# Kernel tuning notes

Measured on AMD Instinct MI355X. Metric: run time of the kernel, lower is better.

The kernel has to match this reference:

```python
import jax, jax.numpy as jnp
import numpy as np

B, S, D, H = 2, 2048, 1024, 16
HD = D // H
WIN = 32
LN_EPS = 1e-5


def _ln(x, g, b):
    m = jnp.mean(x, axis=-1, keepdims=True)
    v = jnp.mean(jnp.square(x - m), axis=-1, keepdims=True)
    return (x - m) / jnp.sqrt(v + LN_EPS) * g + b


def setup_inputs() -> dict:
    key = jax.random.key(0)
    ks = jax.random.split(key, 12)
    def w(k, shape):
        return jax.random.normal(k, shape, dtype=jnp.float32) * 0.02
    inp = {
        'x': jax.random.normal(ks[0], (B, S, D), dtype=jnp.float32),
        'fq_w': w(ks[1], (D, D)), 'fq_b': jnp.zeros((D,), jnp.float32),
        'fk_w': w(ks[2], (D, D)), 'fk_b': jnp.zeros((D,), jnp.float32),
        'fv_w': w(ks[3], (D, D)), 'fv_b': jnp.zeros((D,), jnp.float32),
        'bq_w': w(ks[4], (D, D)), 'bq_b': jnp.zeros((D,), jnp.float32),
        'bk_w': w(ks[5], (D, D)), 'bk_b': jnp.zeros((D,), jnp.float32),
        'bv_w': w(ks[6], (D, D)), 'bv_b': jnp.zeros((D,), jnp.float32),
        'gate_w': w(ks[7], (2 * D, D)), 'gate_b': jnp.zeros((D,), jnp.float32),
        'gln_g': jnp.ones((D,), jnp.float32), 'gln_b': jnp.zeros((D,), jnp.float32),
        'bstr': jnp.asarray(0.1, jnp.float32),
        'out_w': w(ks[8], (D, D)), 'out_b': jnp.zeros((D,), jnp.float32),
        'ln_g': jnp.ones((D,), jnp.float32), 'ln_b': jnp.zeros((D,), jnp.float32),
    }
    return inp


def _heads(x, w, b):
    # [B,S,D] -> [B,H,S,HD]
    y = x @ w + b
    return y.reshape(B, S, H, HD).transpose(0, 2, 1, 3)


def _merge(x):
    return x.transpose(0, 2, 1, 3).reshape(B, S, D)


def _forward(x, fq_w, fq_b, fk_w, fk_b, fv_w, fv_b,
             bq_w, bq_b, bk_w, bk_b, bv_w, bv_b,
             gate_w, gate_b, gln_g, gln_b, bstr, out_w, out_b, ln_g, ln_b):
    scale = 1.0 / np.sqrt(HD)
    i = jnp.arange(S)
    # --- causal forward attention ---
    Q = _heads(x, fq_w, fq_b); K = _heads(x, fk_w, fk_b); V = _heads(x, fv_w, fv_b)
    scores = jnp.einsum('bhqd,bhkd->bhqk', Q, K) * scale
    causal = i[:, None] >= i[None, :]  # allowed positions
    scores = jnp.where(causal[None, None], scores, -jnp.inf)
    fwd = _merge(jnp.einsum('bhqk,bhkd->bhqd', jax.nn.softmax(scores, axis=-1), V))
    # --- limited-window backward attention (future_context = hidden_states) ---
    Qb = _heads(x, bq_w, bq_b); Kb = _heads(x, bk_w, bk_b); Vb = _heads(x, bv_w, bv_b)
    sb = jnp.einsum('bhqd,bhkd->bhqk', Qb, Kb) * scale
    valid = (i[None, :] > i[:, None]) & (i[None, :] <= i[:, None] + WIN)
    sb = jnp.where(valid[None, None], sb, -jnp.inf)
    # rows with no valid future (last row) get scores reset to 0 -> uniform softmax,
    # matching torch's all_masked handling
    row_valid = valid.any(axis=-1)  # [S]
    sb = jnp.where(row_valid[None, None, :, None], sb, 0.0)
    bwd = _merge(jnp.einsum('bhqk,bhkd->bhqd', jax.nn.softmax(sb, axis=-1), Vb))
    # --- weak gated fusion (eval mode: no dropout, backward detached) ---
    combined = jnp.concatenate([fwd, bwd], axis=-1)
    gate = jax.nn.sigmoid(_ln(combined @ gate_w + gate_b, gln_g, gln_b))
    strength = jax.nn.sigmoid(bstr) * 0.3
    fused = fwd + strength * gate * jax.lax.stop_gradient(bwd)
    out = fused @ out_w + out_b
    return _ln(x + out, ln_g, ln_b)


def reference(x, fq_w, fq_b, fk_w, fk_b, fv_w, fv_b,
              bq_w, bq_b, bk_w, bk_b, bv_w, bv_b,
              gate_w, gate_b, gln_g, gln_b, bstr, out_w, out_b, ln_g, ln_b):
    return _forward(x, fq_w, fq_b, fk_w, fk_b, fv_w, fv_b,
                    bq_w, bq_b, bk_w, bk_b, bv_w, bv_b,
                    gate_w, gate_b, gln_g, gln_b, bstr, out_w, out_b, ln_g, ln_b)
```

## Files before the change

kernel.cpp:

```cpp
#include <hip/hip_runtime.h>

#define S_LEN 2048
#define NH 16
#define HD 64
#define DMODEL 1024
#define NTOK 4096
#define ELTS_PER 4194304
#define QSCALE 0.18033688f

typedef __attribute__((ext_vector_type(8))) __bf16 bfrag;
typedef __attribute__((ext_vector_type(8))) short s8v;
typedef __attribute__((ext_vector_type(4))) float f32x4;

__device__ inline float bf2f(short s) {
  unsigned int u = ((unsigned int)(unsigned short)s) << 16;
  float f;
  __builtin_memcpy(&f, &u, 4);
  return f;
}
__device__ inline short f2bf(float f) {
  unsigned int u;
  __builtin_memcpy(&u, &f, 4);
  u = (u + 0x7fffu + ((u >> 16) & 1u)) >> 16;
  return (short)u;
}
__device__ inline short f2bf_n(float f) {
  __bf16 h = (__bf16)f;
  short s;
  __builtin_memcpy(&s, &h, 2);
  return s;
}
__device__ inline float bflo(unsigned int u) {
  unsigned int t = u << 16;
  float f; __builtin_memcpy(&f, &t, 4); return f;
}
__device__ inline float bfhi(unsigned int u) {
  unsigned int t = u & 0xffff0000u;
  float f; __builtin_memcpy(&f, &t, 4); return f;
}
__device__ __forceinline__ void gll16(const short* g, short* l) {
  __builtin_amdgcn_global_load_lds(
      (const __attribute__((address_space(1))) void*)g,
      (__attribute__((address_space(3))) void*)l, 16, 0, 0);
}

__global__ __launch_bounds__(256) void cvt_bf16_kernel(const float* __restrict__ in,
                                                       short* __restrict__ out, int n) {
  int i = (blockIdx.x * 256 + threadIdx.x) * 4;
  if (i + 3 < n) {
    float4 v = *reinterpret_cast<const float4*>(in + i);
    short4 o;
    o.x = f2bf(v.x); o.y = f2bf(v.y); o.z = f2bf(v.z); o.w = f2bf(v.w);
    *reinterpret_cast<short4*>(out + i) = o;
  }
}

__global__ void transpose_cvt_all(const float* __restrict__ s0, const float* __restrict__ s1,
                                  const float* __restrict__ s2, const float* __restrict__ s3,
                                  const float* __restrict__ s4, const float* __restrict__ s5,
                                  const float* __restrict__ s6, const float* __restrict__ s7,
                                  short* d0, short* d1, short* d2, short* d3,
                                  short* d4, short* d5, short* d6, short* d7) {
  const int z = blockIdx.z;
  const int K = (z == 7) ? 2048 : 1024;
  if (blockIdx.y * 32 >= K) return;
  const float* srcs[8] = {s0, s1, s2, s3, s4, s5, s6, s7};
  short* dsts[8] = {d0, d1, d2, d3, d4, d5, d6, d7};
  const float* in = srcs[z];
  short* out = dsts[z];
  __shared__ float tile[32][33];
  int nb = blockIdx.x * 32, kb = blockIdx.y * 32;
  int tx = threadIdx.x, ty = threadIdx.y;
  for (int j = 0; j < 32; j += 8)
    tile[ty + j][tx] = in[(size_t)(kb + ty + j) * 1024 + nb + tx];
  __syncthreads();
  for (int j = 0; j < 32; j += 8)
    out[(size_t)(nb + ty + j) * K + kb + tx] = f2bf(tile[tx][ty + j]);
}

__global__ __launch_bounds__(256) void gemm_qkv_kernel(
    const short* __restrict__ A, int lda, int K,
    const short* __restrict__ B0, const short* __restrict__ B1, const short* __restrict__ B2,
    const short* __restrict__ B3, const short* __restrict__ B4, const short* __restrict__ B5,
    const float* __restrict__ bias0, const float* __restrict__ bias1,
    const float* __restrict__ bias2, const float* __restrict__ bias3,
    const float* __restrict__ bias4, const float* __restrict__ bias5,
    short* __restrict__ outQ) {
  __shared__ short As[128 * 32];
  __shared__ short Bs[128 * 32];
  const int tid = threadIdx.x;
  const int n0 = blockIdx.x * 128;
  const int m0 = blockIdx.y * 128;
  const short* Bp[6] = {B0, B1, B2, B3, B4, B5};
  const float* biasP[6] = {bias0, bias1, bias2, bias3, bias4, bias5};
  const int nsel = n0 >> 10;
  const short* Bt = Bp[nsel] + (size_t)(n0 & 1023) * K;
  const float* bsel = biasP[nsel];

  const int lane = tid & 63;
  const int w = tid >> 6;
  const int wm = (w >> 1) * 64;
  const int wn = (w & 1) * 64;
  const int lr = lane & 15;
  const int lg = lane >> 4;
  const int gr = lane >> 2;
  const int gs = (((lane & 3) ^ ((gr >> 1) & 3)) * 8);
  const int rsw = (lr >> 1) & 3;

  f32x4 acc[4][4];
  for (int a = 0; a < 4; ++a)
    for (int b = 0; b < 4; ++b) acc[a][b] = {0.f, 0.f, 0.f, 0.f};

  for (int k0 = 0; k0 < K; k0 += 32) {
    __syncthreads();
    const short* Ag = A + (size_t)(m0 + w * 32 + gr) * lda + k0 + gs;
    const short* Bg = Bt + (size_t)(w * 32 + gr) * K + k0 + gs;
    gll16(Ag, &As[(w * 32) * 32]);
    gll16(Ag + (size_t)16 * lda, &As[(w * 32 + 16) * 32]);
    gll16(Bg, &Bs[(w * 32) * 32]);
    gll16(Bg + (size_t)16 * K, &Bs[(w * 32 + 16) * 32]);
    __syncthreads();
    bfrag af[4], bfr[4];
    for (int t = 0; t < 4; ++t) {
      af[t] = *reinterpret_cast<const bfrag*>(&As[(wm + t * 16 + lr) * 32 + ((lg ^ rsw) * 8)]);
      bfr[t] = *reinterpret_cast<const bfrag*>(&Bs[(wn + t * 16 + lr) * 32 + ((lg ^ rsw) * 8)]);
    }
    for (int mt = 0; mt < 4; ++mt)
      for (int nt = 0; nt < 4; ++nt)
        acc[mt][nt] = __builtin_amdgcn_mfma_f32_16x16x32_bf16(af[mt], bfr[nt], acc[mt][nt], 0, 0, 0);
  }

  const float cmul = (nsel == 0 || nsel == 3) ? QSCALE : 1.0f;
  for (int mt = 0; mt < 4; ++mt)
    for (int nt = 0; nt < 4; ++nt) {
      int rowb = m0 + wm + mt * 16 + lg * 4;
      int col = n0 + wn + nt * 16 + lr;
      int nh = col & 1023;
      int hh = nh >> 6, d = nh & 63;
      int bb = rowb >> 11, s0 = rowb & 2047;
      float bv = bsel[nh];
      if (nsel == 2 || nsel == 5) {
        short4 o;
        o.x = f2bf_n(acc[mt][nt][0] + bv);
        o.y = f2bf_n(acc[mt][nt][1] + bv);
        o.z = f2bf_n(acc[mt][nt][2] + bv);
        o.w = f2bf_n(acc[mt][nt][3] + bv);
        *reinterpret_cast<short4*>(
            outQ + (size_t)nsel * ELTS_PER +
            ((size_t)(bb * NH + hh) * HD + d) * S_LEN + s0) = o;
      } else {
        for (int i = 0; i < 4; ++i) {
          float v = (acc[mt][nt][i] + bv) * cmul;
          outQ[(size_t)nsel * ELTS_PER +
               (((size_t)(bb * NH + hh) * S_LEN + (s0 + i)) * HD) + d] = f2bf_n(v);
        }
      }
    }
}

__global__ __launch_bounds__(256) void gemm_ksplit_kernel(
    const short* __restrict__ A0, const short* __restrict__ A1, int lda,
    const short* __restrict__ B, int ldb, int K,
    const float* __restrict__ bias, float* __restrict__ out0, float* __restrict__ out1) {
  __shared__ short As[128 * 32];
  __shared__ short Bs[128 * 32];
  const int tid = threadIdx.x;
  const int n0 = blockIdx.x * 128;
  const int m0 = blockIdx.y * 128;
  const int z = blockIdx.z;
  const short* A = z ? A1 : A0;
  const short* Bt = B + (size_t)n0 * ldb + z * K;
  float* outp = z ? out1 : out0;

  const int lane = tid & 63;
  const int w = tid >> 6;
  const int wm = (w >> 1) * 64;
  const int wn = (w & 1) * 64;
  const int lr = lane & 15;
  const int lg = lane >> 4;
  const int gr = lane >> 2;
  const int gs = (((lane & 3) ^ ((gr >> 1) & 3)) * 8);
  const int rsw = (lr >> 1) & 3;

  f32x4 acc[4][4];
  for (int a = 0; a < 4; ++a)
    for (int b = 0; b < 4; ++b) acc[a][b] = {0.f, 0.f, 0.f, 0.f};

  for (int k0 = 0; k0 < K; k0 += 32) {
    __syncthreads();
    const short* Ag = A + (size_t)(m0 + w * 32 + gr) * lda + k0 + gs;
    const short* Bg = Bt + (size_t)(w * 32 + gr) * ldb + k0 + gs;
    gll16(Ag, &As[(w * 32) * 32]);
    gll16(Ag + (size_t)16 * lda, &As[(w * 32 + 16) * 32]);
    gll16(Bg, &Bs[(w * 32) * 32]);
    gll16(Bg + (size_t)16 * ldb, &Bs[(w * 32 + 16) * 32]);
    __syncthreads();
    bfrag af[4], bfr[4];
    for (int t = 0; t < 4; ++t) {
      af[t] = *reinterpret_cast<const bfrag*>(&As[(wm + t * 16 + lr) * 32 + ((lg ^ rsw) * 8)]);
      bfr[t] = *reinterpret_cast<const bfrag*>(&Bs[(wn + t * 16 + lr) * 32 + ((lg ^ rsw) * 8)]);
    }
    for (int mt = 0; mt < 4; ++mt)
      for (int nt = 0; nt < 4; ++nt)
        acc[mt][nt] = __builtin_amdgcn_mfma_f32_16x16x32_bf16(af[mt], bfr[nt], acc[mt][nt], 0, 0, 0);
  }

  for (int mt = 0; mt < 4; ++mt)
    for (int nt = 0; nt < 4; ++nt)
      for (int i = 0; i < 4; ++i) {
        int row = m0 + wm + mt * 16 + lg * 4 + i;
        int col = n0 + wn + nt * 16 + lr;
        float v = acc[mt][nt][i] + (z == 0 ? bias[col] : 0.f);
        outp[(size_t)row * DMODEL + col] = v;
      }
}

__global__ __launch_bounds__(256) void attn_fwd_kernel(const short* __restrict__ Q,
                                                       const short* __restrict__ Kk,
                                                       const short* __restrict__ VT,
                                                       short* __restrict__ fwd) {
  __shared__ short Ps[4][32 * 72];
  const int tid = threadIdx.x;
  const int lane = tid & 63;
  const int w = tid >> 6;
  const int lr = lane & 15;
  const int lg = lane >> 4;
  const int f = blockIdx.x;
  const int xcd = f & 7;
  const int slot = f >> 3;
  const int bh = xcd * 4 + (slot >> 4);
  const int p = slot & 15;
  const int b = bh >> 4;
  const int h = bh & 15;
  const size_t hb = (size_t)(b * NH + h) * S_LEN * HD;
  short* Pw = Ps[w];

  s8v onesi = {0x3F80, 0x3F80, 0x3F80, 0x3F80, 0x3F80, 0x3F80, 0x3F80, 0x3F80};
  bfrag onesv;
  __builtin_memcpy(&onesv, &onesi, 16);

  const int c = (w < 2) ? (2 * p + w) : (63 - 2 * p - (w - 2));
  const int q0 = c * 32;
  const int ktm = c >> 1;

  bfrag qf[2][2];
  for (int mt = 0; mt < 2; ++mt)
    for (int kc = 0; kc < 2; ++kc)
      qf[mt][kc] = *reinterpret_cast<const bfrag*>(
          Q + hb + (size_t)(q0 + mt * 16 + lr) * HD + kc * 32 + lg * 8);

  f32x4 oacc[2][4];
  for (int mt = 0; mt < 2; ++mt)
    for (int nd = 0; nd < 4; ++nd) oacc[mt][nd] = {0.f, 0.f, 0.f, 0.f};
  f32x4 osum[2];
  osum[0] = {0.f, 0.f, 0.f, 0.f};
  osum[1] = {0.f, 0.f, 0.f, 0.f};

  bfrag ka[4][2];
  for (int nb = 0; nb < 4; ++nb)
    for (int kc = 0; kc < 2; ++kc)
      ka[nb][kc] = *reinterpret_cast<const bfrag*>(
          Kk + hb + (size_t)(nb * 16 + lr) * HD + kc * 32 + lg * 8);

  for (int kt = 0; kt <= ktm; ++kt) {
    bfrag vf[4][2];
    for (int nd = 0; nd < 4; ++nd)
      for (int kc = 0; kc < 2; ++kc)
        vf[nd][kc] = *reinterpret_cast<const bfrag*>(
            VT + hb + (size_t)(nd * 16 + lr) * S_LEN + kt * 64 + kc * 32 + lg * 8);
    f32x4 sv[2][4];
    for (int mt = 0; mt < 2; ++mt)
      for (int nb = 0; nb < 4; ++nb) {
        f32x4 z = {0.f, 0.f, 0.f, 0.f};
        z = __builtin_amdgcn_mfma_f32_16x16x32_bf16(qf[mt][0], ka[nb][0], z, 0, 0, 0);
        sv[mt][nb] = __builtin_amdgcn_mfma_f32_16x16x32_bf16(qf[mt][1], ka[nb][1], z, 0, 0, 0);
      }
    if (kt < ktm) {
      for (int nb = 0; nb < 4; ++nb)
        for (int kc = 0; kc < 2; ++kc)
          ka[nb][kc] = *reinterpret_cast<const bfrag*>(
              Kk + hb + (size_t)((kt + 1) * 64 + nb * 16 + lr) * HD + kc * 32 + lg * 8);
    }
    if (kt == ktm) {
      for (int mt = 0; mt < 2; ++mt)
        for (int nb = 0; nb < 4; ++nb)
          for (int i = 0; i < 4; ++i) {
            int colg = kt * 64 + nb * 16 + lr;
            int rowg = q0 + mt * 16 + lg * 4 + i;
            if (colg > rowg) sv[mt][nb][i] = -1e30f;
          }
    }
    for (int mt = 0; mt < 2; ++mt)
      for (int nb = 0; nb < 4; ++nb)
        for (int i = 0; i < 4; ++i)
          Pw[(mt * 16 + lg * 4 + i) * 72 + nb * 16 + lr] = f2bf_n(exp2f(sv[mt][nb][i]));
    for (int mt = 0; mt < 2; ++mt) {
      bfrag pa0 = *reinterpret_cast<const bfrag*>(&Pw[(mt * 16 + lr) * 72 + lg * 8]);
      bfrag pa1 = *reinterpret_cast<const bfrag*>(&Pw[(mt * 16 + lr) * 72 + 32 + lg * 8]);
      for (int nd = 0; nd < 4; ++nd) {
        oacc[mt][nd] = __builtin_amdgcn_mfma_f32_16x16x32_bf16(pa0, vf[nd][0], oacc[mt][nd], 0, 0, 0);
        oacc[mt][nd] = __builtin_amdgcn_mfma_f32_16x16x32_bf16(pa1, vf[nd][1], oacc[mt][nd], 0, 0, 0);
      }
      osum[mt] = __builtin_amdgcn_mfma_f32_16x16x32_bf16(pa0, onesv, osum[mt], 0, 0, 0);
      osum[mt] = __builtin_amdgcn_mfma_f32_16x16x32_bf16(pa1, onesv, osum[mt], 0, 0, 0);
    }
  }

  for (int mt = 0; mt < 2; ++mt)
    for (int i = 0; i < 4; ++i) {
      int rowg = q0 + mt * 16 + lg * 4 + i;
      float inv = 1.0f / osum[mt][i];
      for (int nd = 0; nd < 4; ++nd)
        fwd[(size_t)(b * S_LEN + rowg) * DMODEL + h * HD + nd * 16 + lr] =
            f2bf(oacc[mt][nd][i] * inv);
    }
}

__global__ __launch_bounds__(256) void attn_bwd_kernel(const short* __restrict__ Qb,
                                                       const short* __restrict__ Kb,
                                                       const short* __restrict__ VT,
                                                       short* __restrict__ bwd) {
  __shared__ short Ps[4][32 * 72];
  const int tid = threadIdx.x;
  const int lane = tid & 63;
  const int w = tid >> 6;
  const int lr = lane & 15;
  const int lg = lane >> 4;
  const int h = blockIdx.y;
  const int b = blockIdx.z;
  const size_t hb = (size_t)(b * NH + h) * S_LEN * HD;
  const int q0 = blockIdx.x * 128 + w * 32;
  short* Pw = Ps[w];

  bfrag qf[2][2];
  for (int mt = 0; mt < 2; ++mt)
    for (int kc = 0; kc < 2; ++kc)
      qf[mt][kc] = *reinterpret_cast<const bfrag*>(
          Qb + hb + (size_t)(q0 + mt * 16 + lr) * HD + kc * 32 + lg * 8);
  bfrag kf[4][2];
  for (int nb = 0; nb < 4; ++nb) {
    int kr = q0 + nb * 16 + lr;
    kr = min(kr, S_LEN - 1);
    for (int kc = 0; kc < 2; ++kc)
      kf[nb][kc] = *reinterpret_cast<const bfrag*>(
          Kb + hb + (size_t)kr * HD + kc * 32 + lg * 8);
  }
  f32x4 sv[2][4];
  for (int mt = 0; mt < 2; ++mt)
    for (int nb = 0; nb < 4; ++nb) {
      f32x4 z = {0.f, 0.f, 0.f, 0.f};
      z = __builtin_amdgcn_mfma_f32_16x16x32_bf16(qf[mt][0], kf[nb][0], z, 0, 0, 0);
      sv[mt][nb] = __builtin_amdgcn_mfma_f32_16x16x32_bf16(qf[mt][1], kf[nb][1], z, 0, 0, 0);
    }
  float mx[2][4];
  for (int mt = 0; mt < 2; ++mt)
    for (int i = 0; i < 4; ++i) {
      int rowg = q0 + mt * 16 + lg * 4 + i;
      float m = -1e30f;
      for (int nb = 0; nb < 4; ++nb) {
        int colg = q0 + nb * 16 + lr;
        float t = sv[mt][nb][i];
        bool valid = (colg > rowg) && (colg <= rowg + 32) && (colg < S_LEN);
        if (!valid) t = -1e30f;
        sv[mt][nb][i] = t;
        m = fmaxf(m, t);
      }
      mx[mt][i] = m;
    }
  for (int off = 1; off < 16; off <<= 1)
    for (int mt = 0; mt < 2; ++mt)
      for (int i = 0; i < 4; ++i) mx[mt][i] = fmaxf(mx[mt][i], __shfl_xor(mx[mt][i], off));
  float rs[2][4] = {{0.f, 0.f, 0.f, 0.f}, {0.f, 0.f, 0.f, 0.f}};
  for (int mt = 0; mt < 2; ++mt)
    for (int nb = 0; nb < 4; ++nb)
      for (int i = 0; i < 4; ++i) {
        float p = exp2f(sv[mt][nb][i] - mx[mt][i]);
        rs[mt][i] += p;
        Pw[(mt * 16 + lg * 4 + i) * 72 + nb * 16 + lr] = f2bf_n(p);
      }
  for (int off = 1; off < 16; off <<= 1)
    for (int mt = 0; mt < 2; ++mt)
      for (int i = 0; i < 4; ++i) rs[mt][i] += __shfl_xor(rs[mt][i], off);
  bfrag vf[4][2];
  for (int nd = 0; nd < 4; ++nd)
    for (int kc = 0; kc < 2; ++kc) {
      int sbase = q0 + kc * 32 + lg * 8;
      sbase = min(sbase, S_LEN - 8);
      vf[nd][kc] = *reinterpret_cast<const bfrag*>(
          VT + hb + (size_t)(nd * 16 + lr) * S_LEN + sbase);
    }
  f32x4 oacc[2][4];
  for (int mt = 0; mt < 2; ++mt)
    for (int nd = 0; nd < 4; ++nd) oacc[mt][nd] = {0.f, 0.f, 0.f, 0.f};
  for (int mt = 0; mt < 2; ++mt) {
    bfrag pa0 = *reinterpret_cast<const bfrag*>(&Pw[(mt * 16 + lr) * 72 + lg * 8]);
    bfrag pa1 = *reinterpret_cast<const bfrag*>(&Pw[(mt * 16 + lr) * 72 + 32 + lg * 8]);
    for (int nd = 0; nd < 4; ++nd) {
      oacc[mt][nd] = __builtin_amdgcn_mfma_f32_16x16x32_bf16(pa0, vf[nd][0], oacc[mt][nd], 0, 0, 0);
      oacc[mt][nd] = __builtin_amdgcn_mfma_f32_16x16x32_bf16(pa1, vf[nd][1], oacc[mt][nd], 0, 0, 0);
    }
  }
  for (int mt = 0; mt < 2; ++mt)
    for (int nd = 0; nd < 4; ++nd)
      for (int i = 0; i < 4; ++i) {
        int rowg = q0 + mt * 16 + lg * 4 + i;
        float ov = oacc[mt][nd][i] / rs[mt][i];
        bwd[(size_t)(b * S_LEN + rowg) * DMODEL + h * HD + nd * 16 + lr] = f2bf(ov);
      }
}

__global__ __launch_bounds__(256) void vmean_kernel(const short* __restrict__ VT,
                                                    short* __restrict__ bwd) {
  __shared__ float red[256];
  const int bh = blockIdx.x;
  const int d = threadIdx.x >> 2;
  const int seg = threadIdx.x & 3;
  const short* row = VT + (size_t)bh * S_LEN * HD + (size_t)d * S_LEN + seg * 512;
  float s = 0.f;
  for (int j = 0; j < 512; j += 8) {
    uint4 v = *reinterpret_cast<const uint4*>(row + j);
    s += bflo(v.x) + bfhi(v.x) + bflo(v.y) + bfhi(v.y) +
         bflo(v.z) + bfhi(v.z) + bflo(v.w) + bfhi(v.w);
  }
  red[threadIdx.x] = s;
  __syncthreads();
  if (seg == 0) {
    float t = red[d * 4] + red[d * 4 + 1] + red[d * 4 + 2] + red[d * 4 + 3];
    int b = bh >> 4, h = bh & 15;
    bwd[((size_t)(b * S_LEN + S_LEN - 1)) * DMODEL + h * HD + d] = f2bf(t * (1.f / S_LEN));
  }
}

__global__ __launch_bounds__(256) void ln_gate_fuse_kernel(
    const float* __restrict__ g0p, const float* __restrict__ g1p,
    const float* __restrict__ gln_g, const float* __restrict__ gln_b,
    const short* __restrict__ fwd, const short* __restrict__ bwd,
    const float* __restrict__ bstr, short* __restrict__ fused) {
  __shared__ float red[8];
  const int row = blockIdx.x;
  const int tid = threadIdx.x;
  const int lane = tid & 63;
  const int w = tid >> 6;
  float4 x0 = *reinterpret_cast<const float4*>(g0p + (size_t)row * DMODEL + tid * 4);
  float4 x1 = *reinterpret_cast<const float4*>(g1p + (size_t)row * DMODEL + tid * 4);
  float xa[4] = {x0.x + x1.x, x0.y + x1.y, x0.z + x1.z, x0.w + x1.w};
  float s = xa[0] + xa[1] + xa[2] + xa[3];
  float ss = xa[0] * xa[0] + xa[1] * xa[1] + xa[2] * xa[2] + xa[3] * xa[3];
  for (int off = 1; off < 64; off <<= 1) {
    s += __shfl_xor(s, off);
    ss += __shfl_xor(ss, off);
  }
  if (lane == 0) { red[w] = s; red[4 + w] = ss; }
  __syncthreads();
  s = red[0] + red[1] + red[2] + red[3];
  ss = red[4] + red[5] + red[6] + red[7];
  const float mean = s * (1.f / DMODEL);
  const float var = ss * (1.f / DMODEL) - mean * mean;
  const float rstd = rsqrtf(var + 1e-5f);
  const float strength = 0.3f / (1.f + __expf(-bstr[0]));
  for (int e = 0; e < 4; ++e) {
    int idx = tid * 4 + e;
    float g = (xa[e] - mean) * rstd * gln_g[idx] + gln_b[idx];
    float gate = 1.f / (1.f + __expf(-g));
    float f = bf2f(fwd[(size_t)row * DMODEL + idx]) +
              strength * gate * bf2f(bwd[(size_t)row * DMODEL + idx]);
    fused[(size_t)row * DMODEL + idx] = f2bf(f);
  }
}

__global__ __launch_bounds__(256) void final_ln_kernel(const float* __restrict__ x,
                                                       const float* __restrict__ o0p,
                                                       const float* __restrict__ o1p,
                                                       const float* __restrict__ ln_g,
                                                       const float* __restrict__ ln_b,
                                                       float* __restrict__ y) {
  __shared__ float red[8];
  const int row = blockIdx.x;
  const int tid = threadIdx.x;
  const int lane = tid & 63;
  const int w = tid >> 6;
  float4 xv = *reinterpret_cast<const float4*>(x + (size_t)row * DMODEL + tid * 4);
  float4 o0 = *reinterpret_cast<const float4*>(o0p + (size_t)row * DMODEL + tid * 4);
  float4 o1 = *reinterpret_cast<const float4*>(o1p + (size_t)row * DMODEL + tid * 4);
  float t[4] = {xv.x + o0.x + o1.x, xv.y + o0.y + o1.y,
                xv.z + o0.z + o1.z, xv.w + o0.w + o1.w};
  float s = t[0] + t[1] + t[2] + t[3];
  float ss = t[0] * t[0] + t[1] * t[1] + t[2] * t[2] + t[3] * t[3];
  for (int off = 1; off < 64; off <<= 1) {
    s += __shfl_xor(s, off);
    ss += __shfl_xor(ss, off);
  }
  if (lane == 0) { red[w] = s; red[4 + w] = ss; }
  __syncthreads();
  s = red[0] + red[1] + red[2] + red[3];
  ss = red[4] + red[5] + red[6] + red[7];
  const float mean = s * (1.f / DMODEL);
  const float var = ss * (1.f / DMODEL) - mean * mean;
  const float rstd = rsqrtf(var + 1e-5f);
  for (int e = 0; e < 4; ++e) {
    int idx = tid * 4 + e;
    y[(size_t)row * DMODEL + idx] = (t[e] - mean) * rstd * ln_g[idx] + ln_b[idx];
  }
}

extern "C" void kernel_launch(void* const* d_in, const int* in_sizes, int n_in,
                              void* d_out, int out_size, void* d_ws, size_t ws_size,
                              hipStream_t stream) {
  const float* x = (const float*)d_in[0];
  const float* fq_w = (const float*)d_in[1];
  const float* fq_b = (const float*)d_in[2];
  const float* fk_w = (const float*)d_in[3];
  const float* fk_b = (const float*)d_in[4];
  const float* fv_w = (const float*)d_in[5];
  const float* fv_b = (const float*)d_in[6];
  const float* bq_w = (const float*)d_in[7];
  const float* bq_b = (const float*)d_in[8];
  const float* bk_w = (const float*)d_in[9];
  const float* bk_b = (const float*)d_in[10];
  const float* bv_w = (const float*)d_in[11];
  const float* bv_b = (const float*)d_in[12];
  const float* gate_w = (const float*)d_in[13];
  const float* gate_b = (const float*)d_in[14];
  const float* gln_g = (const float*)d_in[15];
  const float* gln_b = (const float*)d_in[16];
  const float* bstr = (const float*)d_in[17];
  const float* out_w = (const float*)d_in[18];
  const float* out_b = (const float*)d_in[19];
  const float* ln_g = (const float*)d_in[20];
  const float* ln_b = (const float*)d_in[21];

  char* ws = (char*)d_ws;
  const size_t MB = 1u << 20;
  short* xb = (short*)(ws + 0);
  short* wT0 = (short*)(ws + 8 * MB);
  short* wT1 = (short*)(ws + 10 * MB);
  short* wT2 = (short*)(ws + 12 * MB);
  short* wT3 = (short*)(ws + 14 * MB);
  short* wT4 = (short*)(ws + 16 * MB);
  short* wT5 = (short*)(ws + 18 * MB);
  short* gwT = (short*)(ws + 20 * MB);
  short* owT = (short*)(ws + 24 * MB);
  short* qkv = (short*)(ws + 26 * MB);
  short* fwd = (short*)(ws + 0);
  short* bwdb = (short*)(ws + 8 * MB);
  float* G0 = (float*)(ws + 26 * MB);
  float* G1 = (float*)(ws + 42 * MB);
  short* fused = (short*)(ws + 58 * MB);
  float* O0 = (float*)(ws + 26 * MB);
  float* O1 = (float*)(ws + 42 * MB);

  cvt_bf16_kernel<<<4096, 256, 0, stream>>>(x, xb, ELTS_PER);
  transpose_cvt_all<<<dim3(32, 64, 8), dim3(32, 8), 0, stream>>>(
      fq_w, fk_w, fv_w, bq_w, bk_w, bv_w, out_w, gate_w,
      wT0, wT1, wT2, wT3, wT4, wT5, owT, gwT);

  gemm_qkv_kernel<<<dim3(48, 32), 256, 0, stream>>>(
      xb, 1024, 1024, wT0, wT1, wT2, wT3, wT4, wT5,
      fq_b, fk_b, fv_b, bq_b, bk_b, bv_b, qkv);

  attn_fwd_kernel<<<512, 256, 0, stream>>>(
      qkv, qkv + (size_t)ELTS_PER, qkv + 2 * (size_t)ELTS_PER, fwd);
  attn_bwd_kernel<<<dim3(16, 16, 2), 256, 0, stream>>>(
      qkv + 3 * (size_t)ELTS_PER, qkv + 4 * (size_t)ELTS_PER, qkv + 5 * (size_t)ELTS_PER, bwdb);
  vmean_kernel<<<32, 256, 0, stream>>>(qkv + 5 * (size_t)ELTS_PER, bwdb);

  gemm_ksplit_kernel<<<dim3(8, 32, 2), 256, 0, stream>>>(
      fwd, bwdb, 1024, gwT, 2048, 1024, gate_b, G0, G1);

  ln_gate_fuse_kernel<<<4096, 256, 0, stream>>>(G0, G1, gln_g, gln_b, fwd, bwdb, bstr, fused);

  gemm_ksplit_kernel<<<dim3(8, 32, 2), 256, 0, stream>>>(
      fused, fused + 512, 1024, owT, 1024, 512, out_b, O0, O1);

  final_ln_kernel<<<4096, 256, 0, stream>>>(x, O0, O1, ln_g, ln_b, (float*)d_out);
}
```

Measured before the change: 276.7 us.

## Double GEMM K-tile to 64 and stage QKV epilogue through LDS for vector stores

Both GEMM kernels now load a 64-wide K slice per iteration with a new 8-way XOR swizzle, which halves the number of barrier pairs per K loop. The QKV projection epilogue now writes results into a padded LDS buffer, transposed for the V outputs, and then emits 16-byte vectorized stores to the head-major Q/K and transposed V layouts. This replaces the scattered 2-byte and 8-byte global stores. In exchange it uses more LDS per block, which may reduce occupancy, and adds an extra barrier and LDS round trip.

```diff
diff --git a/kernel.cpp b/kernel.cpp
--- a/kernel.cpp
+++ b/kernel.cpp
@@ -86,15 +86,17 @@
     const float* __restrict__ bias2, const float* __restrict__ bias3,
     const float* __restrict__ bias4, const float* __restrict__ bias5,
     short* __restrict__ outQ) {
-  __shared__ short As[128 * 32];
-  __shared__ short Bs[128 * 32];
+  __shared__ short lds[128 * 136];
+  short* As = lds;
+  short* Bs = lds + 8192;
   const int tid = threadIdx.x;
   const int n0 = blockIdx.x * 128;
   const int m0 = blockIdx.y * 128;
   const short* Bp[6] = {B0, B1, B2, B3, B4, B5};
   const float* biasP[6] = {bias0, bias1, bias2, bias3, bias4, bias5};
   const int nsel = n0 >> 10;
-  const short* Bt = Bp[nsel] + (size_t)(n0 & 1023) * K;
+  const int nc0 = n0 & 1023;
+  const short* Bt = Bp[nsel] + (size_t)nc0 * K;
   const float* bsel = biasP[nsel];
 
   const int lane = tid & 63;
@@ -103,67 +105,78 @@
   const int wn = (w & 1) * 64;
   const int lr = lane & 15;
   const int lg = lane >> 4;
-  const int gr = lane >> 2;
-  const int gs = (((lane & 3) ^ ((gr >> 1) & 3)) * 8);
-  const int rsw = (lr >> 1) & 3;
+  const int rl = lane >> 3;
+  const int gch = (lane & 7) ^ (rl & 7);
 
   f32x4 acc[4][4];
   for (int a = 0; a < 4; ++a)
     for (int b = 0; b < 4; ++b) acc[a][b] = {0.f, 0.f, 0.f, 0.f};
 
-  for (int k0 = 0; k0 < K; k0 += 32) {
+  for (int k0 = 0; k0 < K; k0 += 64) {
     __syncthreads();
-    const short* Ag = A + (size_t)(m0 + w * 32 + gr) * lda + k0 + gs;
-    const short* Bg = Bt + (size_t)(w * 32 + gr) * K + k0 + gs;
-    gll16(Ag, &As[(w * 32) * 32]);
-    gll16(Ag + (size_t)16 * lda, &As[(w * 32 + 16) * 32]);
-    gll16(Bg, &Bs[(w * 32) * 32]);
-    gll16(Bg + (size_t)16 * K, &Bs[(w * 32 + 16) * 32]);
+    for (int p = 0; p < 4; ++p) {
+      int rb = (p * 4 + w) * 8;
+      gll16(A + (size_t)(m0 + rb + rl) * lda + k0 + gch * 8, &As[rb * 64]);
+      gll16(Bt + (size_t)(rb + rl) * K + k0 + gch * 8, &Bs[rb * 64]);
+    }
     __syncthreads();
-    bfrag af[4], bfr[4];
-    for (int t = 0; t < 4; ++t) {
-      af[t] = *reinterpret_cast<const bfrag*>(&As[(wm + t * 16 + lr) * 32 + ((lg ^ rsw) * 8)]);
-      bfr[t] = *reinterpret_cast<const bfrag*>(&Bs[(wn + t * 16 + lr) * 32 + ((lg ^ rsw) * 8)]);
-    }
-    for (int mt = 0; mt < 4; ++mt)
-      for (int nt = 0; nt < 4; ++nt)
-        acc[mt][nt] = __builtin_amdgcn_mfma_f32_16x16x32_bf16(af[mt], bfr[nt], acc[mt][nt], 0, 0, 0);
+    for (int ks = 0; ks < 2; ++ks) {
+      bfrag af[4], bf[4];
+      for (int t = 0; t < 4; ++t) {
+        af[t] = *reinterpret_cast<const bfrag*>(
+            &As[(wm + t * 16 + lr) * 64 + (((lg + 4 * ks) ^ (lr & 7)) * 8)]);
+        bf[t] = *reinterpret_cast<const bfrag*>(
+            &Bs[(wn + t * 16 + lr) * 64 + (((lg + 4 * ks) ^ (lr & 7)) * 8)]);
+      }
+      for (int mt = 0; mt < 4; ++mt)
+        for (int nt = 0; nt < 4; ++nt)
+          acc[mt][nt] = __builtin_amdgcn_mfma_f32_16x16x32_bf16(af[mt], bf[nt], acc[mt][nt], 0, 0, 0);
+    }
   }
 
   const float cmul = (nsel == 0 || nsel == 3) ? QSCALE : 1.0f;
+  const bool tr = (nsel == 2 || nsel == 5);
+  __syncthreads();
   for (int mt = 0; mt < 4; ++mt)
     for (int nt = 0; nt < 4; ++nt) {
-      int rowb = m0 + wm + mt * 16 + lg * 4;
-      int col = n0 + wn + nt * 16 + lr;
-      int nh = col & 1023;
-      int hh = nh >> 6, d = nh & 63;
-      int bb = rowb >> 11, s0 = rowb & 2047;
-      float bv = bsel[nh];
-      if (nsel == 2 || nsel == 5) {
-        short4 o;
-        o.x = f2bf_n(acc[mt][nt][0] + bv);
-        o.y = f2bf_n(acc[mt][nt][1] + bv);
-        o.z = f2bf_n(acc[mt][nt][2] + bv);
-        o.w = f2bf_n(acc[mt][nt][3] + bv);
-        *reinterpret_cast<short4*>(
-            outQ + (size_t)nsel * ELTS_PER +
-            ((size_t)(bb * NH + hh) * HD + d) * S_LEN + s0) = o;
-      } else {
-        for (int i = 0; i < 4; ++i) {
-          float v = (acc[mt][nt][i] + bv) * cmul;
-          outQ[(size_t)nsel * ELTS_PER +
-               (((size_t)(bb * NH + hh) * S_LEN + (s0 + i)) * HD) + d] = f2bf_n(v);
-        }
-      }
-    }
+      int c = wn + nt * 16 + lr;
+      float bv = bsel[nc0 + c];
+      for (int i = 0; i < 4; ++i) {
+        int r = wm + mt * 16 + lg * 4 + i;
+        short v16 = f2bf_n((acc[mt][nt][i] + bv) * cmul);
+        if (tr) lds[c * 136 + r] = v16;
+        else lds[r * 136 + c] = v16;
+      }
+    }
+  __syncthreads();
+  const int bb = m0 >> 11;
+  const int sloc = m0 & 2047;
+  const int hh0 = nc0 >> 6;
+  short* basebuf = outQ + (size_t)nsel * ELTS_PER;
+  for (int j = 0; j < 8; ++j) {
+    int gid = j * 256 + tid;
+    int rr = gid >> 4;
+    int ch = gid & 15;
+    s8v v = *reinterpret_cast<const s8v*>(&lds[rr * 136 + ch * 8]);
+    if (tr) {
+      int hh = hh0 + (rr >> 6), d = rr & 63;
+      *reinterpret_cast<s8v*>(
+          basebuf + ((size_t)(bb * NH + hh) * HD + d) * S_LEN + sloc + ch * 8) = v;
+    } else {
+      int hh = hh0 + (ch >> 3), d0 = (ch & 7) * 8;
+      *reinterpret_cast<s8v*>(
+          basebuf + ((size_t)(bb * NH + hh) * S_LEN + sloc + rr) * HD + d0) = v;
+    }
+  }
 }
 
 __global__ __launch_bounds__(256) void gemm_ksplit_kernel(
     const short* __restrict__ A0, const short* __restrict__ A1, int lda,
     const short* __restrict__ B, int ldb, int K,
     const float* __restrict__ bias, float* __restrict__ out0, float* __restrict__ out1) {
-  __shared__ short As[128 * 32];
-  __shared__ short Bs[128 * 32];
+  __shared__ short lds[16384];
+  short* As = lds;
+  short* Bs = lds + 8192;
   const int tid = threadIdx.x;
   const int n0 = blockIdx.x * 128;
   const int m0 = blockIdx.y * 128;
@@ -178,31 +191,33 @@
   const int wn = (w & 1) * 64;
   const int lr = lane & 15;
   const int lg = lane >> 4;
-  const int gr = lane >> 2;
-  const int gs = (((lane & 3) ^ ((gr >> 1) & 3)) * 8);
-  const int rsw = (lr >> 1) & 3;
+  const int rl = lane >> 3;
+  const int gch = (lane & 7) ^ (rl & 7);
 
   f32x4 acc[4][4];
   for (int a = 0; a < 4; ++a)
     for (int b = 0; b < 4; ++b) acc[a][b] = {0.f, 0.f, 0.f, 0.f};
 
-  for (int k0 = 0; k0 < K; k0 += 32) {
+  for (int k0 = 0; k0 < K; k0 += 64) {
     __syncthreads();
-    const short* Ag = A + (size_t)(m0 + w * 32 + gr) * lda + k0 + gs;
-    const short* Bg = Bt + (size_t)(w * 32 + gr) * ldb + k0 + gs;
-    gll16(Ag, &As[(w * 32) * 32]);
-    gll16(Ag + (size_t)16 * lda, &As[(w * 32 + 16) * 32]);
-    gll16(Bg, &Bs[(w * 32) * 32]);
-    gll16(Bg + (size_t)16 * ldb, &Bs[(w * 32 + 16) * 32]);
+    for (int p = 0; p < 4; ++p) {
+      int rb = (p * 4 + w) * 8;
+      gll16(A + (size_t)(m0 + rb + rl) * lda + k0 + gch * 8, &As[rb * 64]);
+      gll16(Bt + (size_t)(rb + rl) * ldb + k0 + gch * 8, &Bs[rb * 64]);
+    }
     __syncthreads();
-    bfrag af[4], bfr[4];
-    for (int t = 0; t < 4; ++t) {
-      af[t] = *reinterpret_cast<const bfrag*>(&As[(wm + t * 16 + lr) * 32 + ((lg ^ rsw) * 8)]);
-      bfr[t] = *reinterpret_cast<const bfrag*>(&Bs[(wn + t * 16 + lr) * 32 + ((lg ^ rsw) * 8)]);
-    }
-    for (int mt = 0; mt < 4; ++mt)
-      for (int nt = 0; nt < 4; ++nt)
-        acc[mt][nt] = __builtin_amdgcn_mfma_f32_16x16x32_bf16(af[mt], bfr[nt], acc[mt][nt], 0, 0, 0);
+    for (int ks = 0; ks < 2; ++ks) {
+      bfrag af[4], bf[4];
+      for (int t = 0; t < 4; ++t) {
+        af[t] = *reinterpret_cast<const bfrag*>(
+            &As[(wm + t * 16 + lr) * 64 + (((lg + 4 * ks) ^ (lr & 7)) * 8)]);
+        bf[t] = *reinterpret_cast<const bfrag*>(
+            &Bs[(wn + t * 16 + lr) * 64 + (((lg + 4 * ks) ^ (lr & 7)) * 8)]);
+      }
+      for (int mt = 0; mt < 4; ++mt)
+        for (int nt = 0; nt < 4; ++nt)
+          acc[mt][nt] = __builtin_amdgcn_mfma_f32_16x16x32_bf16(af[mt], bf[nt], acc[mt][nt], 0, 0, 0);
+    }
   }
 
   for (int mt = 0; mt < 4; ++mt)
```

Result: faster. 264.0 us (-4.6%).
